# Kernel tuning notes

Hardware: AMD Instinct MI355X
Metric: run time of the kernel (lower is better)

The kernel has to match this reference:

```python
import jax, jax.numpy as jnp
import numpy as np
from jax.scipy.linalg import cho_solve

N, D, K, M = 2048, 128, 8, 64
JITTER = 1e-5


def setup_inputs() -> dict:
    key = jax.random.key(0)
    ks = jax.random.split(key, 5)
    X = jax.random.normal(ks[0], (N, D), jnp.float32)
    Y = jax.random.normal(ks[1], (N, 1), jnp.float32)
    q_mu = 0.1 * jax.random.normal(ks[2], (K, D), jnp.float32)
    # positive variational covariances ~ 1/D, as in the original init
    q_cov = jax.random.uniform(ks[3], (K, D), jnp.float32, 0.5 / D, 1.5 / D)
    Z = jax.random.normal(ks[4], (M, K), jnp.float32)
    sigma_f = jnp.float32(1.0)
    noise_var = jnp.float32(0.01)
    return {"X": X, "Y": Y, "q_mu": q_mu, "q_cov": q_cov, "Z": Z,
            "sigma_f": sigma_f, "noise_var": noise_var}


def _compute_psi1(X, q_mu, q_cov, Z, sigma_f):
    # q_mu_X: (K, N)
    q_mu_X = jnp.einsum('kd,nd->kn', q_mu, X)
    # top: (K, N, M)
    top = (q_mu_X[:, :, None] - Z.T[:, None, :]) ** 2
    # bot: (K, N)
    bot = 1.0 + jnp.einsum('kd,nd->kn', q_cov, X * X)
    bot = bot[:, :, None]
    psi1 = jnp.exp(-0.5 * top / bot) / jnp.sqrt(bot)  # (K, N, M)
    return sigma_f * jnp.prod(psi1, axis=0)  # (N, M)


def _compute_batched_psi2(X, q_mu, q_cov, Z, sigma_f):
    q_mu_X = jnp.einsum('kd,nd->kn', q_mu, X)  # (K, N)
    Z_diff = Z[:, None, :] - Z[None, :, :]      # (M, M, K)
    Z_bar = 0.5 * (Z[:, None, :] + Z[None, :, :])  # (M, M, K)
    # top: (K, N, M, M) -- the dominant intermediate
    top = (q_mu_X[:, :, None, None] - jnp.transpose(Z_bar, (2, 0, 1))[:, None, :, :]) ** 2
    bot = 2.0 * jnp.einsum('kd,nd->kn', q_cov, X * X) + 1.0  # (K, N)
    bot = bot[:, :, None, None]
    right = jnp.prod(jnp.exp(-top / bot) / jnp.sqrt(bot), axis=0)  # (N, M, M)
    left = (sigma_f ** 2) * jnp.exp(-0.25 * jnp.sum(Z_diff ** 2, axis=2))  # (M, M)
    return left * right  # (N, M, M)


def _rbf_K(Z):
    # ARD RBF with unit variance and unit lengthscales (frozen in original)
    sq = jnp.sum((Z[:, None, :] - Z[None, :, :]) ** 2, axis=-1)
    return jnp.exp(-0.5 * sq)


def _chol_logdet(chol):
    return 2.0 * jnp.sum(jnp.log(jnp.diagonal(chol)), axis=-1)


def _elbo(X, Y, q_mu, q_cov, Z, sigma_f, noise_var):
    n = X.shape[0]
    d = X.shape[1]
    m = Z.shape[0]
    sigma2 = jnp.reshape(noise_var, ())
    sf = jnp.reshape(sigma_f, ())
    two_pi = jnp.asarray(2.0 * np.pi, X.dtype)
    eye = jnp.eye(m, dtype=X.dtype)

    Kuu = _rbf_K(Z) + eye * JITTER
    chol_Ku = jnp.linalg.cholesky(Kuu)
    F1 = -n * jnp.log(two_pi) - (n - m) * jnp.log(sigma2) + _chol_logdet(chol_Ku)

    YY = Y.T @ Y  # (1, 1)
    psi2 = jnp.sum(_compute_batched_psi2(X, q_mu, q_cov, Z, sf), axis=0)  # (M, M)
    Ku_Psi2 = sigma2 * Kuu + psi2 + eye * JITTER
    chol_Ku_Psi2 = jnp.linalg.cholesky(Ku_Psi2)
    F1 = F1 - _chol_logdet(chol_Ku_Psi2) - YY / sigma2  # (1, 1)

    psi1 = _compute_psi1(X, q_mu, q_cov, Z, sf)  # (N, M)
    Psi1_Y = psi1.T @ Y  # (M, 1)
    F1 = F1 + (Psi1_Y.T @ cho_solve((chol_Ku_Psi2, True), Psi1_Y)) / sigma2

    psi0 = n * sf ** 2
    KuiPsi2 = cho_solve((chol_Ku, True), psi2)
    F1 = F1 - psi0 / sigma2 + jnp.trace(KuiPsi2) / sigma2

    KL = jnp.sum(jnp.log(q_cov), axis=1)
    KL = KL - d * jnp.log(jnp.sum(q_cov + q_mu ** 2, axis=1))
    KL = KL + d * jnp.asarray(np.log(d), X.dtype)
    KL = jnp.sum(KL)
    return jnp.squeeze(0.5 * (F1 + KL))


def reference(X, Y, q_mu, q_cov, Z, sigma_f, noise_var):
    return _elbo(X, Y, q_mu, q_cov, Z, sigma_f, noise_var)
```

## Files before the change

### kernel.cpp

```cpp
#include <hip/hip_runtime.h>
#include <math.h>

namespace {
constexpr int N_ = 2048;
constexpr int D_ = 128;
constexpr int K_ = 8;
constexpr int M_ = 64;
constexpr float JIT = 1e-5f;
constexpr float L2E = 1.4426950408889634f;
constexpr float LN2 = 0.6931471805599453f;

constexpr int OFF_ARR2 = 0;
constexpr int OFF_C2   = N_ * 16;
constexpr int OFF_P2P  = N_ * 17;
constexpr int OFF_P1Y  = N_ * 17 + 16 * 4096;
}

struct F8 { float f[8]; };

__device__ __forceinline__ float f4e(float4 v, int e) {
  return (e == 0) ? v.x : (e == 1) ? v.y : (e == 2) ? v.z : v.w;
}

__global__ __launch_bounds__(256) void vdmgp_prep_p1y(
    const float* __restrict__ X, const float* __restrict__ Y,
    const float* __restrict__ qmu, const float* __restrict__ qcov,
    const float* __restrict__ Z, float* __restrict__ ws) {
  __shared__ float smu[D_ * K_];
  __shared__ float scov[D_ * K_];
  __shared__ float sa1[256 * 16];
  __shared__ float scy[256];
  __shared__ float red[256];
  const int tid = threadIdx.x;
  for (int idx = tid; idx < K_ * D_; idx += 256) {
    int k = idx >> 7, d = idx & 127;
    smu[d * K_ + k]  = qmu[idx];
    scov[d * K_ + k] = qcov[idx];
  }
  __syncthreads();

  const int n = blockIdx.x * 256 + tid;
  float a[K_], s2[K_];
#pragma unroll
  for (int k = 0; k < K_; k++) { a[k] = 0.f; s2[k] = 0.f; }

  const float4* xrow = reinterpret_cast<const float4*>(X + n * D_);
  for (int dq = 0; dq < D_ / 4; dq++) {
    float4 xv = xrow[dq];
    float xs[4] = {xv.x, xv.y, xv.z, xv.w};
#pragma unroll
    for (int t = 0; t < 4; t++) {
      const int d = dq * 4 + t;
      const float x = xs[t];
      const float xx = x * x;
      F8 mu = *reinterpret_cast<const F8*>(&smu[d * K_]);
      F8 cv = *reinterpret_cast<const F8*>(&scov[d * K_]);
#pragma unroll
      for (int k = 0; k < K_; k++) {
        a[k]  = fmaf(mu.f[k], x, a[k]);
        s2[k] = fmaf(cv.f[k], xx, s2[k]);
      }
    }
  }

  float4 w2[4];
  float prod2 = 1.f, prod1 = 1.f;
#pragma unroll
  for (int k = 0; k < K_; k++) {
    const float b2 = 2.f * s2[k] + 1.f;
    const float b1 = 1.f + s2[k];
    reinterpret_cast<float*>(w2)[k]     = a[k];
    reinterpret_cast<float*>(w2)[8 + k] = L2E / b2;
    sa1[tid * 16 + k]     = a[k];
    sa1[tid * 16 + 8 + k] = 0.5f * L2E / b1;
    prod2 *= rsqrtf(b2);
    prod1 *= rsqrtf(b1);
  }
  float4* arr2q = reinterpret_cast<float4*>(ws + OFF_ARR2 + n * 16);
#pragma unroll
  for (int e = 0; e < 4; e++) arr2q[e] = w2[e];
  (ws + OFF_C2)[n] = prod2;
  scy[tid] = prod1 * Y[n];
  __syncthreads();

  const int m = tid & 63;
  const int stripe = tid >> 6;
  float zm[K_];
#pragma unroll
  for (int k = 0; k < K_; k++) zm[k] = Z[m * K_ + k];

  float acc = 0.f;
  for (int t = 0; t < 64; t++) {
    const int nl = stripe * 64 + t;
    const F8 av = *reinterpret_cast<const F8*>(&sa1[nl * 16]);
    const F8 ib = *reinterpret_cast<const F8*>(&sa1[nl * 16 + 8]);
    float s = 0.f;
#pragma unroll
    for (int k = 0; k < K_; k++) {
      const float d = av.f[k] - zm[k];
      s = fmaf(d * d, ib.f[k], s);
    }
    acc = fmaf(scy[nl], exp2f(-s), acc);
  }
  red[tid] = acc;
  __syncthreads();
  if (tid < 64)
    (ws + OFF_P1Y)[blockIdx.x * 64 + tid] =
        red[tid] + red[64 + tid] + red[128 + tid] + red[192 + tid];
}

__global__ __launch_bounds__(256) void vdmgp_psi2(
    const float* __restrict__ Z, const float* __restrict__ ws,
    float* __restrict__ part) {
  __shared__ float sa[128 * 16];
  __shared__ float sc[128];
  const int tid = threadIdx.x;
  const int pair = blockIdx.x * 256 + tid;
  const int i = pair >> 6, j = pair & 63;

  float zb[K_];
#pragma unroll
  for (int k = 0; k < K_; k++) zb[k] = 0.5f * (Z[i * K_ + k] + Z[j * K_ + k]);

  const int nbase = blockIdx.y * 128;
  const float4* src = reinterpret_cast<const float4*>(ws + OFF_ARR2 + nbase * 16);
  float4* dst = reinterpret_cast<float4*>(sa);
  for (int idx = tid; idx < 128 * 4; idx += 256) dst[idx] = src[idx];
  if (tid < 128) sc[tid] = (ws + OFF_C2)[nbase + tid];
  __syncthreads();

  float acc = 0.f;
  for (int nl = 0; nl < 128; nl++) {
    const F8 av = *reinterpret_cast<const F8*>(&sa[nl * 16]);
    const F8 ib = *reinterpret_cast<const F8*>(&sa[nl * 16 + 8]);
    float s = 0.f;
#pragma unroll
    for (int k = 0; k < K_; k++) {
      const float t = av.f[k] - zb[k];
      s = fmaf(t * t, ib.f[k], s);
    }
    acc = fmaf(sc[nl], exp2f(-s), acc);
  }
  part[blockIdx.y * 4096 + pair] = acc;
}

__global__ __launch_bounds__(256, 1) void vdmgp_final(
    const float* __restrict__ Y,
    const float* __restrict__ qmu, const float* __restrict__ qcov,
    const float* __restrict__ Z,
    const float* __restrict__ sfp, const float* __restrict__ nvp,
    const float* __restrict__ ws, float* __restrict__ out) {
  __shared__ float P2s[M_][M_];
  __shared__ float zl[M_][9];
  __shared__ float pysL[M_];
  __shared__ __align__(16) float rowbuf[2][2][2][M_];
  __shared__ float scal[8];

  const int tid = threadIdx.x;
  const int lane = tid & 63;
  const int wave = tid >> 6;
  const float sf = sfp[0];
  const float s2v = nvp[0];

  for (int idx = tid; idx < M_ * K_; idx += 256) zl[idx >> 3][idx & 7] = Z[idx];
  if (tid < M_) {
    const float* p1y = ws + OFF_P1Y;
    float s = 0.f;
#pragma unroll
    for (int b = 0; b < 8; b++) s += p1y[b * M_ + tid];
    pysL[tid] = sf * s;
  }
  __syncthreads();

  const float4* part4 = reinterpret_cast<const float4*>(ws + OFF_P2P);
  const float sf2 = sf * sf;
#pragma unroll
  for (int g = 0; g < 4; g++) {
    const int idx4 = g * 256 + tid;
    float4 acc = {0.f, 0.f, 0.f, 0.f};
#pragma unroll
    for (int c = 0; c < 16; c++) {
      const float4 v = part4[c * 1024 + idx4];
      acc.x += v.x; acc.y += v.y; acc.z += v.z; acc.w += v.w;
    }
    const int i = idx4 >> 4;
    const int j0 = (idx4 & 15) * 4;
    float o[4];
#pragma unroll
    for (int e = 0; e < 4; e++) {
      const int j = j0 + e;
      float sq = 0.f;
#pragma unroll
      for (int k = 0; k < K_; k++) {
        const float dd = zl[i][k] - zl[j][k];
        sq = fmaf(dd, dd, sq);
      }
      o[e] = sf2 * exp2f(-0.25f * L2E * sq) * f4e(acc, e);
    }
    *reinterpret_cast<float4*>(&P2s[i][j0]) = make_float4(o[0], o[1], o[2], o[3]);
  }
  __syncthreads();

  if (wave < 2) {
    const bool isA2 = (wave == 1);
    float zj[K_];
#pragma unroll
    for (int k = 0; k < K_; k++) zj[k] = zl[lane][k];

    float reg[M_];
#pragma unroll
    for (int i = 0; i < M_; i++) {
      float sq = 0.f;
#pragma unroll
      for (int k = 0; k < K_; k++) { const float dd = zl[i][k] - zj[k]; sq = fmaf(dd, dd, sq); }
      const float jit = (i == lane) ? JIT : 0.f;
      const float kj = exp2f(-0.5f * L2E * sq) + jit;
      reg[i] = isA2 ? fmaf(s2v, kj, P2s[i][lane] + jit) : kj;
    }

    float ld = 0.f;
#pragma unroll
    for (int p = 0; p < M_; p += 2) {
      const int par = (p >> 1) & 1;
      float* rbA = rowbuf[wave][par][0];
      float* rbB = rowbuf[wave][par][1];
      rbA[lane] = reg[p];
      rbB[lane] = reg[p + 1];
      float4 ra[16], rb[16];
      const float4* rbAq = reinterpret_cast<const float4*>(rbA);
      const float4* rbBq = reinterpret_cast<const float4*>(rbB);
#pragma unroll
      for (int q = 0; q < 16; q++) { ra[q] = rbAq[q]; rb[q] = rbBq[q]; }

      const float P00 = f4e(ra[p >> 2], p & 3);
      const float P01 = f4e(ra[(p + 1) >> 2], (p + 1) & 3);
      const float P11 = f4e(rb[(p + 1) >> 2], (p + 1) & 3);
      const float det = fmaf(P00, P11, -P01 * P01);
      const float idet = __builtin_amdgcn_rcpf(det);
      ld += __log2f(det);
      const float Pi00 =  P11 * idet;
      const float Pi01 = -P01 * idet;
      const float Pi11 =  P00 * idet;

      const bool isp = (lane == p), isq = (lane == p + 1);
      const float a0 = reg[p], a1 = reg[p + 1];
      const float w0 = isp ? Pi00 : (isq ? Pi01 : fmaf(Pi00, a0, Pi01 * a1));
      const float w1 = isp ? Pi01 : (isq ? Pi11 : fmaf(Pi01, a0, Pi11 * a1));
      const float t0 = isp ? (1.f - w0) : (isq ? -w0 : w0);
      const float t1 = isq ? (1.f - w1) : (isp ? -w1 : w1);
      const float f0 = (isp || isq) ? -w0 : w0;
      const float f1 = (isp || isq) ? -w1 : w1;
#pragma unroll
      for (int q = 0; q < 16; q++) {
        const float4 va = ra[q], vb = rb[q];
        reg[4 * q + 0] = fmaf(-t1, vb.x, fmaf(-t0, va.x, reg[4 * q + 0]));
        reg[4 * q + 1] = fmaf(-t1, vb.y, fmaf(-t0, va.y, reg[4 * q + 1]));
        reg[4 * q + 2] = fmaf(-t1, vb.z, fmaf(-t0, va.z, reg[4 * q + 2]));
        reg[4 * q + 3] = fmaf(-t1, vb.w, fmaf(-t0, va.w, reg[4 * q + 3]));
      }
      reg[p] = f0;
      reg[p + 1] = f1;
    }

    float local = 0.f;
    if (!isA2) {
#pragma unroll
      for (int i = 0; i < M_; i++) local = fmaf(reg[i], P2s[i][lane], local);
    } else {
#pragma unroll
      for (int i = 0; i < M_; i++) local = fmaf(reg[i], pysL[i], local);
      local *= pysL[lane];
    }
#pragma unroll
    for (int off = 32; off > 0; off >>= 1) local += __shfl_down(local, off, 64);
    if (lane == 0) {
      scal[4 + 2 * wave] = LN2 * ld;
      scal[5 + 2 * wave] = -local;
    }
  } else {
    const int w = wave - 2;
    float yy = 0.f;
#pragma unroll
    for (int t = 0; t < 16; t++) {
      const float y = Y[w * 1024 + t * 64 + lane];
      yy = fmaf(y, y, yy);
    }
#pragma unroll
    for (int off = 32; off > 0; off >>= 1) yy += __shfl_down(yy, off, 64);
    if (lane == 0) scal[w] = yy;

    const int r = lane >> 4;
    const int k = w * 4 + r;
    const int d0 = (lane & 15) * 8;
    float slog = 0.f, srow = 0.f;
#pragma unroll
    for (int t = 0; t < 8; t++) {
      const float qc = qcov[k * D_ + d0 + t];
      const float qm = qmu[k * D_ + d0 + t];
      slog += logf(qc);
      srow += qc + qm * qm;
    }
#pragma unroll
    for (int off = 8; off > 0; off >>= 1) {
      slog += __shfl_down(slog, off, 16);
      srow += __shfl_down(srow, off, 16);
    }
    float klr = ((lane & 15) == 0)
        ? (slog - (float)D_ * logf(srow) + (float)D_ * logf((float)D_)) : 0.f;
#pragma unroll
    for (int off = 32; off > 0; off >>= 1) klr += __shfl_down(klr, off, 64);
    if (lane == 0) scal[2 + w] = klr;
  }
  __syncthreads();

  if (tid == 0) {
    const float YY = scal[0] + scal[1];
    const float KL = scal[2] + scal[3];
    const float ld1 = scal[4], tr = scal[5], ld2 = scal[6], quad = scal[7];
    const float inv = 1.0f / s2v;
    const float F1 = -(float)N_ * 1.8378770664093453f
                   - (float)(N_ - M_) * logf(s2v)
                   + (ld1 - ld2)
                   - YY * inv
                   + quad * inv
                   - (float)N_ * sf * sf * inv
                   + tr * inv;
    out[0] = 0.5f * (F1 + KL);
  }
}

extern "C" void kernel_launch(void* const* d_in, const int* in_sizes, int n_in,
                              void* d_out, int out_size, void* d_ws, size_t ws_size,
                              hipStream_t stream) {
  const float* X    = (const float*)d_in[0];
  const float* Y    = (const float*)d_in[1];
  const float* qmu  = (const float*)d_in[2];
  const float* qcov = (const float*)d_in[3];
  const float* Z    = (const float*)d_in[4];
  const float* sfp  = (const float*)d_in[5];
  const float* nvp  = (const float*)d_in[6];
  float* ws  = (float*)d_ws;
  float* out = (float*)d_out;

  vdmgp_prep_p1y<<<8, 256, 0, stream>>>(X, Y, qmu, qcov, Z, ws);
  vdmgp_psi2<<<dim3(16, 16), 256, 0, stream>>>(Z, ws, ws + OFF_P2P);
  vdmgp_final<<<1, 256, 0, stream>>>(Y, qmu, qcov, Z, sfp, nvp, ws, out);
}
```

Baseline: 59.91 us.

## Fuse prep, psi1 and psi2 into one grid kernel and precompute Kuu inverse

Merges the per-point statistics kernel into the psi2 and psi1 blocks of a single heterogeneous grid, so each block recomputes its own chunk of X statistics instead of reading them from workspace written by a separate launch. One block also runs the Kuu sweep, YY and KL terms concurrently and stores Kuu^-1 in workspace, which leaves only one 64x64 sweep in the final single-block kernel. This removes a launch and shortens the serial tail. The cost is that the X statistics are computed redundantly 16 times per chunk across the psi2 blocks, and that work now sits on each block's critical path.

```diff
diff --git a/kernel.cpp b/kernel.cpp
--- a/kernel.cpp
+++ b/kernel.cpp
@@ -10,10 +10,10 @@
 constexpr float L2E = 1.4426950408889634f;
 constexpr float LN2 = 0.6931471805599453f;
 
-constexpr int OFF_ARR2 = 0;
-constexpr int OFF_C2   = N_ * 16;
-constexpr int OFF_P2P  = N_ * 17;
-constexpr int OFF_P1Y  = N_ * 17 + 16 * 4096;
+constexpr int OFF_P2P = 0;
+constexpr int OFF_P1Y = 16 * 4096;
+constexpr int OFF_KUI = OFF_P1Y + 1024;
+constexpr int OFF_SC  = OFF_KUI + 4096;
 }
 
 struct F8 { float f[8]; };
@@ -22,28 +22,11 @@
   return (e == 0) ? v.x : (e == 1) ? v.y : (e == 2) ? v.z : v.w;
 }
 
-__global__ __launch_bounds__(256) void vdmgp_prep_p1y(
-    const float* __restrict__ X, const float* __restrict__ Y,
-    const float* __restrict__ qmu, const float* __restrict__ qcov,
-    const float* __restrict__ Z, float* __restrict__ ws) {
-  __shared__ float smu[D_ * K_];
-  __shared__ float scov[D_ * K_];
-  __shared__ float sa1[256 * 16];
-  __shared__ float scy[256];
-  __shared__ float red[256];
-  const int tid = threadIdx.x;
-  for (int idx = tid; idx < K_ * D_; idx += 256) {
-    int k = idx >> 7, d = idx & 127;
-    smu[d * K_ + k]  = qmu[idx];
-    scov[d * K_ + k] = qcov[idx];
-  }
-  __syncthreads();
-
-  const int n = blockIdx.x * 256 + tid;
-  float a[K_], s2[K_];
+__device__ __forceinline__ void compute_stats(
+    const float* __restrict__ X, const float* smu, const float* scov,
+    int n, float* a, float* s2) {
 #pragma unroll
   for (int k = 0; k < K_; k++) { a[k] = 0.f; s2[k] = 0.f; }
-
   const float4* xrow = reinterpret_cast<const float4*>(X + n * D_);
   for (int dq = 0; dq < D_ / 4; dq++) {
     float4 xv = xrow[dq];
@@ -62,98 +45,228 @@
       }
     }
   }
-
-  float4 w2[4];
-  float prod2 = 1.f, prod1 = 1.f;
-#pragma unroll
-  for (int k = 0; k < K_; k++) {
-    const float b2 = 2.f * s2[k] + 1.f;
-    const float b1 = 1.f + s2[k];
-    reinterpret_cast<float*>(w2)[k]     = a[k];
-    reinterpret_cast<float*>(w2)[8 + k] = L2E / b2;
-    sa1[tid * 16 + k]     = a[k];
-    sa1[tid * 16 + 8 + k] = 0.5f * L2E / b1;
-    prod2 *= rsqrtf(b2);
-    prod1 *= rsqrtf(b1);
-  }
-  float4* arr2q = reinterpret_cast<float4*>(ws + OFF_ARR2 + n * 16);
-#pragma unroll
-  for (int e = 0; e < 4; e++) arr2q[e] = w2[e];
-  (ws + OFF_C2)[n] = prod2;
-  scy[tid] = prod1 * Y[n];
-  __syncthreads();
-
-  const int m = tid & 63;
-  const int stripe = tid >> 6;
-  float zm[K_];
-#pragma unroll
-  for (int k = 0; k < K_; k++) zm[k] = Z[m * K_ + k];
-
-  float acc = 0.f;
-  for (int t = 0; t < 64; t++) {
-    const int nl = stripe * 64 + t;
-    const F8 av = *reinterpret_cast<const F8*>(&sa1[nl * 16]);
-    const F8 ib = *reinterpret_cast<const F8*>(&sa1[nl * 16 + 8]);
-    float s = 0.f;
-#pragma unroll
-    for (int k = 0; k < K_; k++) {
-      const float d = av.f[k] - zm[k];
-      s = fmaf(d * d, ib.f[k], s);
-    }
-    acc = fmaf(scy[nl], exp2f(-s), acc);
-  }
-  red[tid] = acc;
-  __syncthreads();
-  if (tid < 64)
-    (ws + OFF_P1Y)[blockIdx.x * 64 + tid] =
-        red[tid] + red[64 + tid] + red[128 + tid] + red[192 + tid];
-}
-
-__global__ __launch_bounds__(256) void vdmgp_psi2(
-    const float* __restrict__ Z, const float* __restrict__ ws,
-    float* __restrict__ part) {
+}
+
+__device__ __forceinline__ float sweep2x2(float* reg, float (*rowbuf)[M_], int lane) {
+  float ld = 0.f;
+#pragma unroll
+  for (int p = 0; p < M_; p += 2) {
+    const int par = (p >> 1) & 1;
+    float* rbA = rowbuf[par * 2 + 0];
+    float* rbB = rowbuf[par * 2 + 1];
+    rbA[lane] = reg[p];
+    rbB[lane] = reg[p + 1];
+    float4 ra[16], rb[16];
+    const float4* rbAq = reinterpret_cast<const float4*>(rbA);
+    const float4* rbBq = reinterpret_cast<const float4*>(rbB);
+#pragma unroll
+    for (int q = 0; q < 16; q++) { ra[q] = rbAq[q]; rb[q] = rbBq[q]; }
+
+    const float P00 = f4e(ra[p >> 2], p & 3);
+    const float P01 = f4e(ra[(p + 1) >> 2], (p + 1) & 3);
+    const float P11 = f4e(rb[(p + 1) >> 2], (p + 1) & 3);
+    const float det = fmaf(P00, P11, -P01 * P01);
+    const float idet = __builtin_amdgcn_rcpf(det);
+    ld += __log2f(det);
+    const float Pi00 =  P11 * idet;
+    const float Pi01 = -P01 * idet;
+    const float Pi11 =  P00 * idet;
+
+    const bool isp = (lane == p), isq = (lane == p + 1);
+    const float a0 = reg[p], a1 = reg[p + 1];
+    const float w0 = isp ? Pi00 : (isq ? Pi01 : fmaf(Pi00, a0, Pi01 * a1));
+    const float w1 = isp ? Pi01 : (isq ? Pi11 : fmaf(Pi01, a0, Pi11 * a1));
+    const float t0 = isp ? (1.f - w0) : (isq ? -w0 : w0);
+    const float t1 = isq ? (1.f - w1) : (isp ? -w1 : w1);
+    const float f0 = (isp || isq) ? -w0 : w0;
+    const float f1 = (isp || isq) ? -w1 : w1;
+#pragma unroll
+    for (int q = 0; q < 16; q++) {
+      const float4 va = ra[q], vb = rb[q];
+      reg[4 * q + 0] = fmaf(-t1, vb.x, fmaf(-t0, va.x, reg[4 * q + 0]));
+      reg[4 * q + 1] = fmaf(-t1, vb.y, fmaf(-t0, va.y, reg[4 * q + 1]));
+      reg[4 * q + 2] = fmaf(-t1, vb.z, fmaf(-t0, va.z, reg[4 * q + 2]));
+      reg[4 * q + 3] = fmaf(-t1, vb.w, fmaf(-t0, va.w, reg[4 * q + 3]));
+    }
+    reg[p] = f0;
+    reg[p + 1] = f1;
+  }
+  return ld;
+}
+
+__global__ __launch_bounds__(256, 1) void vdmgp_mega(
+    const float* __restrict__ X, const float* __restrict__ Y,
+    const float* __restrict__ qmu, const float* __restrict__ qcov,
+    const float* __restrict__ Z, float* __restrict__ ws) {
+  __shared__ float smu[D_ * K_];
+  __shared__ float scov[D_ * K_];
   __shared__ float sa[128 * 16];
   __shared__ float sc[128];
+  __shared__ float red[256];
+  __shared__ float zl[M_][9];
+  __shared__ __align__(16) float rowbuf[4][M_];
+
   const int tid = threadIdx.x;
-  const int pair = blockIdx.x * 256 + tid;
-  const int i = pair >> 6, j = pair & 63;
-
-  float zb[K_];
-#pragma unroll
-  for (int k = 0; k < K_; k++) zb[k] = 0.5f * (Z[i * K_ + k] + Z[j * K_ + k]);
-
-  const int nbase = blockIdx.y * 128;
-  const float4* src = reinterpret_cast<const float4*>(ws + OFF_ARR2 + nbase * 16);
-  float4* dst = reinterpret_cast<float4*>(sa);
-  for (int idx = tid; idx < 128 * 4; idx += 256) dst[idx] = src[idx];
-  if (tid < 128) sc[tid] = (ws + OFF_C2)[nbase + tid];
+  const int bx = blockIdx.x, by = blockIdx.y;
+
+  if (by == 0) {
+    if (bx != 0) return;
+    for (int idx = tid; idx < M_ * K_; idx += 256) zl[idx >> 3][idx & 7] = Z[idx];
+    __syncthreads();
+    const int lane = tid & 63;
+    const int wave = tid >> 6;
+    if (wave == 0) {
+      float zj[K_];
+#pragma unroll
+      for (int k = 0; k < K_; k++) zj[k] = zl[lane][k];
+      float reg[M_];
+#pragma unroll
+      for (int i = 0; i < M_; i++) {
+        float sq = 0.f;
+#pragma unroll
+        for (int k = 0; k < K_; k++) { const float dd = zl[i][k] - zj[k]; sq = fmaf(dd, dd, sq); }
+        reg[i] = exp2f(-0.5f * L2E * sq) + ((i == lane) ? JIT : 0.f);
+      }
+      const float ld = sweep2x2(reg, rowbuf, lane);
+#pragma unroll
+      for (int i = 0; i < M_; i++) ws[OFF_KUI + i * 64 + lane] = reg[i];
+      if (lane == 0) ws[OFF_SC + 2] = LN2 * ld;
+    } else if (wave == 1) {
+      float yy = 0.f;
+#pragma unroll
+      for (int t = 0; t < 32; t++) {
+        const float y = Y[t * 64 + lane];
+        yy = fmaf(y, y, yy);
+      }
+#pragma unroll
+      for (int off = 32; off > 0; off >>= 1) yy += __shfl_down(yy, off, 64);
+      if (lane == 0) ws[OFF_SC + 0] = yy;
+    } else if (wave == 2) {
+      const int k = lane >> 3;
+      const int d0 = (lane & 7) * 16;
+      float slog = 0.f, srow = 0.f;
+#pragma unroll
+      for (int t = 0; t < 16; t++) {
+        const float qc = qcov[k * D_ + d0 + t];
+        const float qm = qmu[k * D_ + d0 + t];
+        slog += logf(qc);
+        srow += qc + qm * qm;
+      }
+#pragma unroll
+      for (int off = 4; off > 0; off >>= 1) {
+        slog += __shfl_down(slog, off, 8);
+        srow += __shfl_down(srow, off, 8);
+      }
+      float klr = ((lane & 7) == 0)
+          ? (slog - (float)D_ * logf(srow) + (float)D_ * logf((float)D_)) : 0.f;
+      klr += __shfl_down(klr, 32, 64);
+      klr += __shfl_down(klr, 16, 64);
+      klr += __shfl_down(klr, 8, 64);
+      if (lane == 0) ws[OFF_SC + 1] = klr;
+    }
+    return;
+  }
+
+  for (int idx = tid; idx < K_ * D_; idx += 256) {
+    int k = idx >> 7, d = idx & 127;
+    smu[d * K_ + k]  = qmu[idx];
+    scov[d * K_ + k] = qcov[idx];
+  }
   __syncthreads();
 
-  float acc = 0.f;
-  for (int nl = 0; nl < 128; nl++) {
-    const F8 av = *reinterpret_cast<const F8*>(&sa[nl * 16]);
-    const F8 ib = *reinterpret_cast<const F8*>(&sa[nl * 16 + 8]);
-    float s = 0.f;
-#pragma unroll
-    for (int k = 0; k < K_; k++) {
-      const float t = av.f[k] - zb[k];
-      s = fmaf(t * t, ib.f[k], s);
-    }
-    acc = fmaf(sc[nl], exp2f(-s), acc);
-  }
-  part[blockIdx.y * 4096 + pair] = acc;
+  if (by <= 16) {
+    const int chunk = by - 1;
+    if (tid < 128) {
+      const int n = chunk * 128 + tid;
+      float a[K_], s2[K_];
+      compute_stats(X, smu, scov, n, a, s2);
+      float prod2 = 1.f;
+#pragma unroll
+      for (int k = 0; k < K_; k++) {
+        const float b2 = 2.f * s2[k] + 1.f;
+        sa[tid * 16 + k]     = a[k];
+        sa[tid * 16 + 8 + k] = L2E / b2;
+        prod2 *= rsqrtf(b2);
+      }
+      sc[tid] = prod2;
+    }
+    __syncthreads();
+
+    const int pair = bx * 256 + tid;
+    const int i = pair >> 6, j = pair & 63;
+    float zb[K_];
+#pragma unroll
+    for (int k = 0; k < K_; k++) zb[k] = 0.5f * (Z[i * K_ + k] + Z[j * K_ + k]);
+
+    float acc = 0.f;
+    for (int nl = 0; nl < 128; nl++) {
+      const F8 av = *reinterpret_cast<const F8*>(&sa[nl * 16]);
+      const F8 ib = *reinterpret_cast<const F8*>(&sa[nl * 16 + 8]);
+      float s = 0.f;
+#pragma unroll
+      for (int k = 0; k < K_; k++) {
+        const float t = av.f[k] - zb[k];
+        s = fmaf(t * t, ib.f[k], s);
+      }
+      acc = fmaf(sc[nl], exp2f(-s), acc);
+    }
+    (ws + OFF_P2P)[chunk * 4096 + pair] = acc;
+    return;
+  }
+
+  {
+    const int chunk = bx;
+    if (tid < 128) {
+      const int n = chunk * 128 + tid;
+      float a[K_], s2[K_];
+      compute_stats(X, smu, scov, n, a, s2);
+      float prod1 = 1.f;
+#pragma unroll
+      for (int k = 0; k < K_; k++) {
+        const float b1 = 1.f + s2[k];
+        sa[tid * 16 + k]     = a[k];
+        sa[tid * 16 + 8 + k] = 0.5f * L2E / b1;
+        prod1 *= rsqrtf(b1);
+      }
+      sc[tid] = prod1 * Y[n];
+    }
+    __syncthreads();
+
+    const int m = tid & 63;
+    const int stripe = tid >> 6;
+    float zm[K_];
+#pragma unroll
+    for (int k = 0; k < K_; k++) zm[k] = Z[m * K_ + k];
+
+    float acc = 0.f;
+    for (int t = 0; t < 32; t++) {
+      const int nl = stripe * 32 + t;
+      const F8 av = *reinterpret_cast<const F8*>(&sa[nl * 16]);
+      const F8 ib = *reinterpret_cast<const F8*>(&sa[nl * 16 + 8]);
+      float s = 0.f;
+#pragma unroll
+      for (int k = 0; k < K_; k++) {
+        const float d = av.f[k] - zm[k];
+        s = fmaf(d * d, ib.f[k], s);
+      }
+      acc = fmaf(sc[nl], exp2f(-s), acc);
+    }
+    red[tid] = acc;
+    __syncthreads();
+    if (tid < 64)
+      (ws + OFF_P1Y)[chunk * 64 + tid] =
+          red[tid] + red[64 + tid] + red[128 + tid] + red[192 + tid];
+  }
 }
 
 __global__ __launch_bounds__(256, 1) void vdmgp_final(
-    const float* __restrict__ Y,
-    const float* __restrict__ qmu, const float* __restrict__ qcov,
     const float* __restrict__ Z,
     const float* __restrict__ sfp, const float* __restrict__ nvp,
     const float* __restrict__ ws, float* __restrict__ out) {
   __shared__ float P2s[M_][M_];
   __shared__ float zl[M_][9];
   __shared__ float pysL[M_];
-  __shared__ __align__(16) float rowbuf[2][2][2][M_];
+  __shared__ __align__(16) float rowbuf[4][M_];
   __shared__ float scal[8];
 
   const int tid = threadIdx.x;
@@ -167,7 +280,7 @@
     const float* p1y = ws + OFF_P1Y;
     float s = 0.f;
 #pragma unroll
-    for (int b = 0; b < 8; b++) s += p1y[b * M_ + tid];
+    for (int c = 0; c < 16; c++) s += p1y[c * M_ + tid];
     pysL[tid] = sf * s;
   }
   __syncthreads();
@@ -201,12 +314,10 @@
   }
   __syncthreads();
 
-  if (wave < 2) {
-    const bool isA2 = (wave == 1);
+  if (wave == 0) {
     float zj[K_];
 #pragma unroll
     for (int k = 0; k < K_; k++) zj[k] = zl[lane][k];
-
     float reg[M_];
 #pragma unroll
     for (int i = 0; i < M_; i++) {
@@ -215,108 +326,35 @@
       for (int k = 0; k < K_; k++) { const float dd = zl[i][k] - zj[k]; sq = fmaf(dd, dd, sq); }
       const float jit = (i == lane) ? JIT : 0.f;
       const float kj = exp2f(-0.5f * L2E * sq) + jit;
-      reg[i] = isA2 ? fmaf(s2v, kj, P2s[i][lane] + jit) : kj;
-    }
-
-    float ld = 0.f;
-#pragma unroll
-    for (int p = 0; p < M_; p += 2) {
-      const int par = (p >> 1) & 1;
-      float* rbA = rowbuf[wave][par][0];
-      float* rbB = rowbuf[wave][par][1];
-      rbA[lane] = reg[p];
-      rbB[lane] = reg[p + 1];
-      float4 ra[16], rb[16];
-      const float4* rbAq = reinterpret_cast<const float4*>(rbA);
-      const float4* rbBq = reinterpret_cast<const float4*>(rbB);
-#pragma unroll
-      for (int q = 0; q < 16; q++) { ra[q] = rbAq[q]; rb[q] = rbBq[q]; }
-
-      const float P00 = f4e(ra[p >> 2], p & 3);
-      const float P01 = f4e(ra[(p + 1) >> 2], (p + 1) & 3);
-      const float P11 = f4e(rb[(p + 1) >> 2], (p + 1) & 3);
-      const float det = fmaf(P00, P11, -P01 * P01);
-      const float idet = __builtin_amdgcn_rcpf(det);
-      ld += __log2f(det);
-      const float Pi00 =  P11 * idet;
-      const float Pi01 = -P01 * idet;
-      const float Pi11 =  P00 * idet;
-
-      const bool isp = (lane == p), isq = (lane == p + 1);
-      const float a0 = reg[p], a1 = reg[p + 1];
-      const float w0 = isp ? Pi00 : (isq ? Pi01 : fmaf(Pi00, a0, Pi01 * a1));
-      const float w1 = isp ? Pi01 : (isq ? Pi11 : fmaf(Pi01, a0, Pi11 * a1));
-      const float t0 = isp ? (1.f - w0) : (isq ? -w0 : w0);
-      const float t1 = isq ? (1.f - w1) : (isp ? -w1 : w1);
-      const float f0 = (isp || isq) ? -w0 : w0;
-      const float f1 = (isp || isq) ? -w1 : w1;
-#pragma unroll
-      for (int q = 0; q < 16; q++) {
-        const float4 va = ra[q], vb = rb[q];
-        reg[4 * q + 0] = fmaf(-t1, vb.x, fmaf(-t0, va.x, reg[4 * q + 0]));
-        reg[4 * q + 1] = fmaf(-t1, vb.y, fmaf(-t0, va.y, reg[4 * q + 1]));
-        reg[4 * q + 2] = fmaf(-t1, vb.z, fmaf(-t0, va.z, reg[4 * q + 2]));
-        reg[4 * q + 3] = fmaf(-t1, vb.w, fmaf(-t0, va.w, reg[4 * q + 3]));
-      }
-      reg[p] = f0;
-      reg[p + 1] = f1;
-    }
-
+      reg[i] = fmaf(s2v, kj, P2s[i][lane] + jit);
+    }
+    const float ld2 = sweep2x2(reg, rowbuf, lane);
     float local = 0.f;
-    if (!isA2) {
-#pragma unroll
-      for (int i = 0; i < M_; i++) local = fmaf(reg[i], P2s[i][lane], local);
-    } else {
-#pragma unroll
-      for (int i = 0; i < M_; i++) local = fmaf(reg[i], pysL[i], local);
-      local *= pysL[lane];
-    }
+#pragma unroll
+    for (int i = 0; i < M_; i++) local = fmaf(reg[i], pysL[i], local);
+    local *= pysL[lane];
 #pragma unroll
     for (int off = 32; off > 0; off >>= 1) local += __shfl_down(local, off, 64);
     if (lane == 0) {
-      scal[4 + 2 * wave] = LN2 * ld;
-      scal[5 + 2 * wave] = -local;
-    }
-  } else {
-    const int w = wave - 2;
-    float yy = 0.f;
-#pragma unroll
-    for (int t = 0; t < 16; t++) {
-      const float y = Y[w * 1024 + t * 64 + lane];
-      yy = fmaf(y, y, yy);
-    }
-#pragma unroll
-    for (int off = 32; off > 0; off >>= 1) yy += __shfl_down(yy, off, 64);
-    if (lane == 0) scal[w] = yy;
-
-    const int r = lane >> 4;
-    const int k = w * 4 + r;
-    const int d0 = (lane & 15) * 8;
-    float slog = 0.f, srow = 0.f;
-#pragma unroll
-    for (int t = 0; t < 8; t++) {
-      const float qc = qcov[k * D_ + d0 + t];
-      const float qm = qmu[k * D_ + d0 + t];
-      slog += logf(qc);
-      srow += qc + qm * qm;
-    }
-#pragma unroll
-    for (int off = 8; off > 0; off >>= 1) {
-      slog += __shfl_down(slog, off, 16);
-      srow += __shfl_down(srow, off, 16);
-    }
-    float klr = ((lane & 15) == 0)
-        ? (slog - (float)D_ * logf(srow) + (float)D_ * logf((float)D_)) : 0.f;
-#pragma unroll
-    for (int off = 32; off > 0; off >>= 1) klr += __shfl_down(klr, off, 64);
-    if (lane == 0) scal[2 + w] = klr;
+      scal[6] = LN2 * ld2;
+      scal[7] = -local;
+    }
+  } else if (wave == 1) {
+    const float* kui = ws + OFF_KUI;
+    float acc = 0.f;
+#pragma unroll
+    for (int i = 0; i < M_; i++) acc = fmaf(kui[i * 64 + lane], P2s[i][lane], acc);
+#pragma unroll
+    for (int off = 32; off > 0; off >>= 1) acc += __shfl_down(acc, off, 64);
+    if (lane == 0) scal[5] = -acc;
   }
   __syncthreads();
 
   if (tid == 0) {
-    const float YY = scal[0] + scal[1];
-    const float KL = scal[2] + scal[3];
-    const float ld1 = scal[4], tr = scal[5], ld2 = scal[6], quad = scal[7];
+    const float YY  = ws[OFF_SC + 0];
+    const float KL  = ws[OFF_SC + 1];
+    const float ld1 = ws[OFF_SC + 2];
+    const float tr = scal[5], ld2 = scal[6], quad = scal[7];
     const float inv = 1.0f / s2v;
     const float F1 = -(float)N_ * 1.8378770664093453f
                    - (float)(N_ - M_) * logf(s2v)
@@ -342,7 +380,6 @@
   float* ws  = (float*)d_ws;
   float* out = (float*)d_out;
 
-  vdmgp_prep_p1y<<<8, 256, 0, stream>>>(X, Y, qmu, qcov, Z, ws);
-  vdmgp_psi2<<<dim3(16, 16), 256, 0, stream>>>(Z, ws, ws + OFF_P2P);
-  vdmgp_final<<<1, 256, 0, stream>>>(Y, qmu, qcov, Z, sfp, nvp, ws, out);
-}
+  vdmgp_mega<<<dim3(16, 18), 256, 0, stream>>>(X, Y, qmu, qcov, Z, ws);
+  vdmgp_final<<<1, 256, 0, stream>>>(Z, sfp, nvp, ws, out);
+}
```

Measured after the change: 62.92 us. 5.0% more time.
